# Optimization experiments

Hardware: AMD Instinct MI355X
Metric: run time of the kernel (lower is better)

The kernel has to match this reference:

```python
import jax, jax.numpy as jnp
import numpy as np

N = 100000
F_IN = 512
HID = 16
N_CLS = 40
E = 3200000


def gcn_conv(x, W, b, src, dst, n_nodes):
    # PyG GCNConv: add self loops, symmetric deg^{-1/2} norm, linear, aggregate.
    loop = jnp.arange(n_nodes, dtype=src.dtype)
    s = jnp.concatenate([src, loop])  # [E+N]
    d = jnp.concatenate([dst, loop])
    deg = jax.ops.segment_sum(jnp.ones_like(d, dtype=x.dtype), d, num_segments=n_nodes)
    dinv = jnp.where(deg > 0, jax.lax.rsqrt(deg), 0.0)
    norm = dinv[s] * dinv[d]  # [E+N]
    h = x @ W  # [N, out] -- transform before propagate (cheaper: out <= in)
    msg = h[s] * norm[:, None]  # gather + scale
    out = jax.ops.segment_sum(msg, d, num_segments=n_nodes)  # scatter-add
    return out + b


def setup_inputs() -> dict:
    key = jax.random.key(0)
    ks = jax.random.split(key, 6)
    x = jax.random.normal(ks[0], (N, F_IN), dtype=jnp.float32)
    edge_index = jax.random.randint(ks[1], (2, E), 0, N, dtype=jnp.int64)
    W1 = jax.random.normal(ks[2], (F_IN, HID), dtype=jnp.float32) / np.sqrt(F_IN)
    b1 = jnp.zeros((HID,), dtype=jnp.float32)
    W2 = jax.random.normal(ks[3], (HID, N_CLS), dtype=jnp.float32) / np.sqrt(HID)
    b2 = jnp.zeros((N_CLS,), dtype=jnp.float32)
    return {"x": x, "edge_index": edge_index, "W1": W1, "b1": b1, "W2": W2, "b2": b2}


def reference(x, edge_index, W1, b1, W2, b2):
    src, dst = edge_index[0], edge_index[1]
    h = gcn_conv(x, W1, b1, src, dst, x.shape[0])
    h = jax.nn.relu(h)
    # dropout: eval mode (identity) for a deterministic reference
    h = gcn_conv(h, W2, b2, src, dst, x.shape[0])
    return jax.nn.log_softmax(h, axis=1)
```

## Files before the change

kernel.cpp:

```cpp
#include <hip/hip_runtime.h>

#define N_NODES 100000
#define NEDGE   3200000
#define F_IN    512
#define HID     16
#define NCLS    40

#define BSHIFT  8
#define BNODES  256
#define NBUCK   ((N_NODES + BNODES - 1) / BNODES)
#define BCAP    8832
#define EPB     5120
#define NPART   (NEDGE / EPB)

typedef __bf16 bf16x8 __attribute__((ext_vector_type(8)));
typedef float floatx4 __attribute__((ext_vector_type(4)));

__global__ __launch_bounds__(256) void k_part(const int* __restrict__ src,
                                              const int* __restrict__ dst,
                                              int* __restrict__ gcnt,
                                              int* __restrict__ ebuf) {
    __shared__ int hist[NBUCK];
    int t = threadIdx.x;
    for (int i = t; i < NBUCK; i += 256) hist[i] = 0;
    __syncthreads();

    int base = blockIdx.x * EPB + t * 4;
    int4 dr[5];
    #pragma unroll
    for (int s = 0; s < 5; s++) {
        dr[s] = *(const int4*)(dst + base + s * 1024);
        atomicAdd(&hist[dr[s].x >> BSHIFT], 1);
        atomicAdd(&hist[dr[s].y >> BSHIFT], 1);
        atomicAdd(&hist[dr[s].z >> BSHIFT], 1);
        atomicAdd(&hist[dr[s].w >> BSHIFT], 1);
    }
    __syncthreads();

    for (int i = t; i < NBUCK; i += 256) {
        int h = hist[i];
        hist[i] = h ? atomicAdd(&gcnt[i], h) : 0;
    }
    __syncthreads();

    #pragma unroll
    for (int s = 0; s < 5; s++) {
        int4 s4 = *(const int4*)(src + base + s * 1024);
        int dd[4] = {dr[s].x, dr[s].y, dr[s].z, dr[s].w};
        int ss[4] = {s4.x, s4.y, s4.z, s4.w};
        #pragma unroll
        for (int j = 0; j < 4; j++) {
            int d = dd[j];
            int b = d >> BSHIFT;
            int p = atomicAdd(&hist[b], 1);
            if (p < BCAP) ebuf[b * BCAP + p] = ((d & (BNODES - 1)) << 17) | ss[j];
        }
    }
}

__global__ __launch_bounds__(256) void k_sortb(const int* __restrict__ gcnt,
                                               const int* __restrict__ ebuf,
                                               int* __restrict__ col,
                                               int* __restrict__ rinfo) {
    __shared__ int ed[BCAP];
    __shared__ int cnt[BNODES];
    __shared__ int pref[BNODES];
    int b = blockIdx.x, t = threadIdx.x;

    int partial = 0;
    for (int i = t; i < b; i += 256) partial += gcnt[i];
    pref[t] = partial;
    __syncthreads();
    for (int off = 128; off; off >>= 1) {
        if (t < off) pref[t] += pref[t + off];
        __syncthreads();
    }
    int gbase = pref[0];
    __syncthreads();

    int ne = gcnt[b];
    if (ne > BCAP) ne = BCAP;
    cnt[t] = 0;
    __syncthreads();
    for (int i = t; i < ne; i += 256) {
        int e = ebuf[b * BCAP + i];
        ed[i] = e;
        atomicAdd(&cnt[e >> 17], 1);
    }
    __syncthreads();
    int c = cnt[t];
    pref[t] = c;
    __syncthreads();
    for (int off = 1; off < 256; off <<= 1) {
        int add = (t >= off) ? pref[t - off] : 0;
        __syncthreads();
        pref[t] += add;
        __syncthreads();
    }
    int start = pref[t] - c;
    int v = b * BNODES + t;
    if (v < N_NODES) rinfo[v] = (c << 22) | (gbase + start);
    cnt[t] = start;
    __syncthreads();
    for (int i = t; i < ne; i += 256) {
        int e = ed[i];
        int pos = atomicAdd(&cnt[e >> 17], 1);
        col[gbase + pos] = e & 0x1FFFF;
    }
}

__global__ __launch_bounds__(256) void k_gemm1(const float* __restrict__ x,
                                               const float* __restrict__ W1,
                                               const int* __restrict__ rinfo,
                                               _Float16* __restrict__ h1s) {
    __shared__ __bf16 wh[16 * 64 * 8];
    __shared__ __bf16 wl[16 * 64 * 8];
    int t = threadIdx.x;
    for (int e = t; e < 8192; e += 256) {
        int c = e >> 9, l = (e >> 3) & 63, j = e & 7;
        int k = c * 32 + ((l >> 4) << 3) + j;
        int n = l & 15;
        float wv = W1[k * HID + n];
        __bf16 h = (__bf16)wv;
        wh[e] = h;
        wl[e] = (__bf16)(wv - (float)h);
    }
    __syncthreads();

    int wave = t >> 6, lane = t & 63;
    int q = lane >> 4, m = lane & 15;
    int row0 = blockIdx.x * 64 + wave * 16;
    int rowa = row0 + m;
    if (rowa >= N_NODES) rowa = N_NODES - 1;
    const float* xr = x + (size_t)rowa * F_IN + q * 8;

    floatx4 acc = {0.f, 0.f, 0.f, 0.f};
    #pragma unroll 4
    for (int c = 0; c < 16; c++) {
        float4 a0 = *(const float4*)(xr + c * 32);
        float4 a1 = *(const float4*)(xr + c * 32 + 4);
        float xv[8] = {a0.x, a0.y, a0.z, a0.w, a1.x, a1.y, a1.z, a1.w};
        bf16x8 ah, al;
        #pragma unroll
        for (int j = 0; j < 8; j++) {
            __bf16 h = (__bf16)xv[j];
            ah[j] = h;
            al[j] = (__bf16)(xv[j] - (float)h);
        }
        bf16x8 bh = *(const bf16x8*)&wh[(c * 64 + lane) * 8];
        bf16x8 bl = *(const bf16x8*)&wl[(c * 64 + lane) * 8];
        acc = __builtin_amdgcn_mfma_f32_16x16x32_bf16(ah, bh, acc, 0, 0, 0);
        acc = __builtin_amdgcn_mfma_f32_16x16x32_bf16(ah, bl, acc, 0, 0, 0);
        acc = __builtin_amdgcn_mfma_f32_16x16x32_bf16(al, bh, acc, 0, 0, 0);
    }
    #pragma unroll
    for (int r = 0; r < 4; r++) {
        int grow = row0 + q * 4 + r;
        if (grow < N_NODES) {
            float dv = rsqrtf((float)(((rinfo[grow] >> 22) & 0x3FF) + 1));
            h1s[grow * HID + (lane & 15)] = (_Float16)(dv * acc[r]);
        }
    }
}

__global__ __launch_bounds__(256) void k_agg1(const _Float16* __restrict__ h1s,
        const int* __restrict__ rinfo, const int* __restrict__ col,
        const float* __restrict__ b1, _Float16* __restrict__ ys) {
    int g = blockIdx.x * 256 + threadIdx.x;
    int v = g >> 4, k = g & 15;
    int ri = rinfo[v];
    int beg = ri & 0x3FFFFF;
    int deg = (ri >> 22) & 0x3FF;
    int end = beg + deg;
    float s0 = 0.f, s1 = 0.f, s2 = 0.f, s3 = 0.f;
    int j = beg;
    for (; j + 7 < end; j += 8) {
        int c0 = col[j],     c1 = col[j + 1], c2 = col[j + 2], c3 = col[j + 3];
        int c4 = col[j + 4], c5 = col[j + 5], c6 = col[j + 6], c7 = col[j + 7];
        s0 += (float)h1s[c0 * HID + k];
        s1 += (float)h1s[c1 * HID + k];
        s2 += (float)h1s[c2 * HID + k];
        s3 += (float)h1s[c3 * HID + k];
        s0 += (float)h1s[c4 * HID + k];
        s1 += (float)h1s[c5 * HID + k];
        s2 += (float)h1s[c6 * HID + k];
        s3 += (float)h1s[c7 * HID + k];
    }
    for (; j < end; j++) s0 += (float)h1s[col[j] * HID + k];
    float sum = (s0 + s1) + (s2 + s3) + (float)h1s[v * HID + k];
    float dv = rsqrtf((float)(deg + 1));
    float val = fmaxf(dv * sum + b1[k], 0.f);
    ys[v * HID + k] = (_Float16)(dv * val);
}

__global__ __launch_bounds__(256) void k_agg2(const _Float16* __restrict__ ys,
        const int* __restrict__ rinfo, const int* __restrict__ col,
        const float* __restrict__ W2, const float* __restrict__ b2,
        float* __restrict__ out) {
    __shared__ float w2s[HID * NCLS];
    __shared__ float b2s[NCLS];
    int t = threadIdx.x;
    for (int i = t; i < HID * NCLS; i += 256) w2s[i] = W2[i];
    if (t < NCLS) b2s[t] = b2[t];
    __syncthreads();

    int g = blockIdx.x * 256 + t;
    int v = g >> 4, l = g & 15;
    int ri = rinfo[v];
    int beg = ri & 0x3FFFFF;
    int deg = (ri >> 22) & 0x3FF;
    int end = beg + deg;
    float s0 = 0.f, s1 = 0.f, s2 = 0.f, s3 = 0.f;
    int j = beg;
    for (; j + 7 < end; j += 8) {
        int c0 = col[j],     c1 = col[j + 1], c2 = col[j + 2], c3 = col[j + 3];
        int c4 = col[j + 4], c5 = col[j + 5], c6 = col[j + 6], c7 = col[j + 7];
        s0 += (float)ys[c0 * HID + l];
        s1 += (float)ys[c1 * HID + l];
        s2 += (float)ys[c2 * HID + l];
        s3 += (float)ys[c3 * HID + l];
        s0 += (float)ys[c4 * HID + l];
        s1 += (float)ys[c5 * HID + l];
        s2 += (float)ys[c6 * HID + l];
        s3 += (float)ys[c7 * HID + l];
    }
    for (; j < end; j++) s0 += (float)ys[col[j] * HID + l];
    float dv = rsqrtf((float)(deg + 1));
    float tval = dv * ((s0 + s1) + (s2 + s3) + (float)ys[v * HID + l]);

    float acc0 = 0.f, acc1 = 0.f, acc2 = 0.f;
    #pragma unroll
    for (int k = 0; k < 16; k++) {
        float tk = __shfl(tval, k, 16);
        acc0 = fmaf(tk, w2s[k * NCLS + l], acc0);
        acc1 = fmaf(tk, w2s[k * NCLS + l + 16], acc1);
        if (l < 8) acc2 = fmaf(tk, w2s[k * NCLS + l + 32], acc2);
    }
    acc0 += b2s[l];
    acc1 += b2s[l + 16];
    float acc2b = (l < 8) ? (acc2 + b2s[l + 32]) : -1e30f;

    float mx = fmaxf(fmaxf(acc0, acc1), acc2b);
    for (int off = 8; off; off >>= 1) mx = fmaxf(mx, __shfl_xor(mx, off, 16));
    float s = __expf(acc0 - mx) + __expf(acc1 - mx) + __expf(acc2b - mx);
    for (int off = 8; off; off >>= 1) s += __shfl_xor(s, off, 16);
    float lse = mx + __logf(s);

    out[v * NCLS + l] = acc0 - lse;
    out[v * NCLS + l + 16] = acc1 - lse;
    if (l < 8) out[v * NCLS + l + 32] = acc2b - lse;
}

extern "C" void kernel_launch(void* const* d_in, const int* in_sizes, int n_in,
                              void* d_out, int out_size, void* d_ws, size_t ws_size,
                              hipStream_t stream) {
    const float* x  = (const float*)d_in[0];
    const int*   ei = (const int*)d_in[1];
    const float* W1 = (const float*)d_in[2];
    const float* b1 = (const float*)d_in[3];
    const float* W2 = (const float*)d_in[4];
    const float* b2 = (const float*)d_in[5];
    float* out = (float*)d_out;
    const int* src = ei;
    const int* dst = ei + NEDGE;

    char* w = (char*)d_ws;
    size_t o = 0;
    auto alloc = [&](size_t bytes) -> char* {
        char* p = w + o;
        o += (bytes + 511) & ~(size_t)511;
        return p;
    };
    int*      gcnt  = (int*)alloc((size_t)NBUCK * 4);
    int*      rinfo = (int*)alloc((size_t)N_NODES * 4);
    int*      col   = (int*)alloc((size_t)NEDGE * 4);
    char*     uni   = alloc((size_t)NBUCK * BCAP * 4);
    int*      ebuf  = (int*)uni;
    _Float16* h1s   = (_Float16*)uni;
    _Float16* ys    = h1s + (size_t)N_NODES * HID;

    hipMemsetAsync(gcnt, 0, (size_t)NBUCK * 4, stream);

    k_part <<<NPART, 256, 0, stream>>>(src, dst, gcnt, ebuf);
    k_sortb<<<NBUCK, 256, 0, stream>>>(gcnt, ebuf, col, rinfo);
    k_gemm1<<<(N_NODES + 63) / 64, 256, 0, stream>>>(x, W1, rinfo, h1s);
    k_agg1 <<<(N_NODES * HID) / 256, 256, 0, stream>>>(h1s, rinfo, col, b1, ys);
    k_agg2 <<<(N_NODES * HID) / 256, 256, 0, stream>>>(ys, rinfo, col, W2, b2, out);
}
```

Baseline: 455.6 us.

## Use 4 threads per node with f16x4 vector gathers in aggregation kernels

Both aggregation kernels now assign four threads per node instead of sixteen, and each thread gathers an 8-byte f16x4 slice of the neighbor row. This cuts the number of col index loads and gather instructions per edge by four, at the cost of more serial work per thread. The second kernel's W2 projection and log-softmax are rebuilt so each thread computes 10 logits, with shuffles over groups of 4 lanes. Per-node output stores become less coalesced, and each thread now needs more registers.

New measurement: 449.0 us. About the same (-1.4%).

```diff
diff --git a/kernel.cpp b/kernel.cpp
--- a/kernel.cpp
+++ b/kernel.cpp
@@ -15,6 +15,7 @@
 
 typedef __bf16 bf16x8 __attribute__((ext_vector_type(8)));
 typedef float floatx4 __attribute__((ext_vector_type(4)));
+typedef _Float16 f16x4 __attribute__((ext_vector_type(4)));
 
 __global__ __launch_bounds__(256) void k_part(const int* __restrict__ src,
                                               const int* __restrict__ dst,
@@ -163,34 +164,45 @@
     }
 }
 
+#define ACC4(gv) { a0 += (float)gv[0]; a1 += (float)gv[1]; \
+                   a2 += (float)gv[2]; a3 += (float)gv[3]; }
+
 __global__ __launch_bounds__(256) void k_agg1(const _Float16* __restrict__ h1s,
         const int* __restrict__ rinfo, const int* __restrict__ col,
         const float* __restrict__ b1, _Float16* __restrict__ ys) {
     int g = blockIdx.x * 256 + threadIdx.x;
-    int v = g >> 4, k = g & 15;
+    int v = g >> 2, q = g & 3;
+    if (v >= N_NODES) return;
     int ri = rinfo[v];
     int beg = ri & 0x3FFFFF;
     int deg = (ri >> 22) & 0x3FF;
     int end = beg + deg;
-    float s0 = 0.f, s1 = 0.f, s2 = 0.f, s3 = 0.f;
+    const f16x4* tab = (const f16x4*)h1s;
+    float a0 = 0.f, a1 = 0.f, a2 = 0.f, a3 = 0.f;
     int j = beg;
     for (; j + 7 < end; j += 8) {
         int c0 = col[j],     c1 = col[j + 1], c2 = col[j + 2], c3 = col[j + 3];
         int c4 = col[j + 4], c5 = col[j + 5], c6 = col[j + 6], c7 = col[j + 7];
-        s0 += (float)h1s[c0 * HID + k];
-        s1 += (float)h1s[c1 * HID + k];
-        s2 += (float)h1s[c2 * HID + k];
-        s3 += (float)h1s[c3 * HID + k];
-        s0 += (float)h1s[c4 * HID + k];
-        s1 += (float)h1s[c5 * HID + k];
-        s2 += (float)h1s[c6 * HID + k];
-        s3 += (float)h1s[c7 * HID + k];
-    }
-    for (; j < end; j++) s0 += (float)h1s[col[j] * HID + k];
-    float sum = (s0 + s1) + (s2 + s3) + (float)h1s[v * HID + k];
+        f16x4 g0 = tab[c0 * 4 + q], g1 = tab[c1 * 4 + q];
+        f16x4 g2 = tab[c2 * 4 + q], g3 = tab[c3 * 4 + q];
+        f16x4 g4 = tab[c4 * 4 + q], g5 = tab[c5 * 4 + q];
+        f16x4 g6 = tab[c6 * 4 + q], g7 = tab[c7 * 4 + q];
+        ACC4(g0) ACC4(g1) ACC4(g2) ACC4(g3)
+        ACC4(g4) ACC4(g5) ACC4(g6) ACC4(g7)
+    }
+    for (; j < end; j++) {
+        f16x4 gv = tab[col[j] * 4 + q];
+        ACC4(gv)
+    }
+    f16x4 sv = tab[v * 4 + q];
+    ACC4(sv)
     float dv = rsqrtf((float)(deg + 1));
-    float val = fmaxf(dv * sum + b1[k], 0.f);
-    ys[v * HID + k] = (_Float16)(dv * val);
+    f16x4 o;
+    o[0] = (_Float16)(dv * fmaxf(dv * a0 + b1[q * 4 + 0], 0.f));
+    o[1] = (_Float16)(dv * fmaxf(dv * a1 + b1[q * 4 + 1], 0.f));
+    o[2] = (_Float16)(dv * fmaxf(dv * a2 + b1[q * 4 + 2], 0.f));
+    o[3] = (_Float16)(dv * fmaxf(dv * a3 + b1[q * 4 + 3], 0.f));
+    ((f16x4*)ys)[v * 4 + q] = o;
 }
 
 __global__ __launch_bounds__(256) void k_agg2(const _Float16* __restrict__ ys,
@@ -205,50 +217,57 @@
     __syncthreads();
 
     int g = blockIdx.x * 256 + t;
-    int v = g >> 4, l = g & 15;
+    int v = g >> 2, q = g & 3;
+    if (v >= N_NODES) return;
     int ri = rinfo[v];
     int beg = ri & 0x3FFFFF;
     int deg = (ri >> 22) & 0x3FF;
     int end = beg + deg;
-    float s0 = 0.f, s1 = 0.f, s2 = 0.f, s3 = 0.f;
+    const f16x4* tab = (const f16x4*)ys;
+    float a0 = 0.f, a1 = 0.f, a2 = 0.f, a3 = 0.f;
     int j = beg;
     for (; j + 7 < end; j += 8) {
         int c0 = col[j],     c1 = col[j + 1], c2 = col[j + 2], c3 = col[j + 3];
         int c4 = col[j + 4], c5 = col[j + 5], c6 = col[j + 6], c7 = col[j + 7];
-        s0 += (float)ys[c0 * HID + l];
-        s1 += (float)ys[c1 * HID + l];
-        s2 += (float)ys[c2 * HID + l];
-        s3 += (float)ys[c3 * HID + l];
-        s0 += (float)ys[c4 * HID + l];
-        s1 += (float)ys[c5 * HID + l];
-        s2 += (float)ys[c6 * HID + l];
-        s3 += (float)ys[c7 * HID + l];
-    }
-    for (; j < end; j++) s0 += (float)ys[col[j] * HID + l];
+        f16x4 g0 = tab[c0 * 4 + q], g1 = tab[c1 * 4 + q];
+        f16x4 g2 = tab[c2 * 4 + q], g3 = tab[c3 * 4 + q];
+        f16x4 g4 = tab[c4 * 4 + q], g5 = tab[c5 * 4 + q];
+        f16x4 g6 = tab[c6 * 4 + q], g7 = tab[c7 * 4 + q];
+        ACC4(g0) ACC4(g1) ACC4(g2) ACC4(g3)
+        ACC4(g4) ACC4(g5) ACC4(g6) ACC4(g7)
+    }
+    for (; j < end; j++) {
+        f16x4 gv = tab[col[j] * 4 + q];
+        ACC4(gv)
+    }
+    f16x4 sv = tab[v * 4 + q];
+    ACC4(sv)
     float dv = rsqrtf((float)(deg + 1));
-    float tval = dv * ((s0 + s1) + (s2 + s3) + (float)ys[v * HID + l]);
-
-    float acc0 = 0.f, acc1 = 0.f, acc2 = 0.f;
+    float tv[4] = {dv * a0, dv * a1, dv * a2, dv * a3};
+
+    float lg[10];
+    #pragma unroll
+    for (int i = 0; i < 10; i++) lg[i] = b2s[q * 10 + i];
     #pragma unroll
     for (int k = 0; k < 16; k++) {
-        float tk = __shfl(tval, k, 16);
-        acc0 = fmaf(tk, w2s[k * NCLS + l], acc0);
-        acc1 = fmaf(tk, w2s[k * NCLS + l + 16], acc1);
-        if (l < 8) acc2 = fmaf(tk, w2s[k * NCLS + l + 32], acc2);
-    }
-    acc0 += b2s[l];
-    acc1 += b2s[l + 16];
-    float acc2b = (l < 8) ? (acc2 + b2s[l + 32]) : -1e30f;
-
-    float mx = fmaxf(fmaxf(acc0, acc1), acc2b);
-    for (int off = 8; off; off >>= 1) mx = fmaxf(mx, __shfl_xor(mx, off, 16));
-    float s = __expf(acc0 - mx) + __expf(acc1 - mx) + __expf(acc2b - mx);
-    for (int off = 8; off; off >>= 1) s += __shfl_xor(s, off, 16);
+        float tk = __shfl(tv[k & 3], k >> 2, 4);
+        #pragma unroll
+        for (int i = 0; i < 10; i++)
+            lg[i] = fmaf(tk, w2s[k * NCLS + q * 10 + i], lg[i]);
+    }
+    float mx = lg[0];
+    #pragma unroll
+    for (int i = 1; i < 10; i++) mx = fmaxf(mx, lg[i]);
+    mx = fmaxf(mx, __shfl_xor(mx, 1, 4));
+    mx = fmaxf(mx, __shfl_xor(mx, 2, 4));
+    float s = 0.f;
+    #pragma unroll
+    for (int i = 0; i < 10; i++) s += __expf(lg[i] - mx);
+    s += __shfl_xor(s, 1, 4);
+    s += __shfl_xor(s, 2, 4);
     float lse = mx + __logf(s);
-
-    out[v * NCLS + l] = acc0 - lse;
-    out[v * NCLS + l + 16] = acc1 - lse;
-    if (l < 8) out[v * NCLS + l + 32] = acc2b - lse;
+    #pragma unroll
+    for (int i = 0; i < 10; i++) out[v * NCLS + q * 10 + i] = lg[i] - lse;
 }
 
 extern "C" void kernel_launch(void* const* d_in, const int* in_sizes, int n_in,
@@ -284,6 +303,6 @@
     k_part <<<NPART, 256, 0, stream>>>(src, dst, gcnt, ebuf);
     k_sortb<<<NBUCK, 256, 0, stream>>>(gcnt, ebuf, col, rinfo);
     k_gemm1<<<(N_NODES + 63) / 64, 256, 0, stream>>>(x, W1, rinfo, h1s);
-    k_agg1 <<<(N_NODES * HID) / 256, 256, 0, stream>>>(h1s, rinfo, col, b1, ys);
-    k_agg2 <<<(N_NODES * HID) / 256, 256, 0, stream>>>(ys, rinfo, col, W2, b2, out);
-}
+    k_agg1 <<<(N_NODES * 4 + 255) / 256, 256, 0, stream>>>(h1s, rinfo, col, b1, ys);
+    k_agg2 <<<(N_NODES * 4 + 255) / 256, 256, 0, stream>>>(ys, rinfo, col, W2, b2, out);
+}
```
